# Optimization experiments

Measured on AMD Instinct MI355X. Metric: run time of the kernel, lower is better.

Reference implementation:

```python
import jax, jax.numpy as jnp
from jax import lax
import numpy as np
import math

DIM = 96      # channels
HEADS = 3     # num_heads
WS = 8        # window size
SHIFT = 4     # window_size // 2 (depth is odd -> shifted)
TLC = 64      # tlc_kernel
H = 264
W = 264


def _grid_idxes(h, w, k1, k2):
    # Faithful replication of the torch grids() tiling index logic (static ints).
    num_row = (h - 1) // k1 + 1
    num_col = (w - 1) // k2 + 1
    step_j = k2 if num_col == 1 else math.ceil((w - k2) / (num_col - 1) - 1e-8)
    step_i = k1 if num_row == 1 else math.ceil((h - k1) / (num_row - 1) - 1e-8)
    idxes = []
    i = 0
    last_i = False
    while i < h and not last_i:
        j = 0
        if i + k1 >= h:
            i = h - k1
            last_i = True
        last_j = False
        while j < w and not last_j:
            if j + k2 >= w:
                j = w - k2
                last_j = True
            idxes.append((i, j))
            j = j + step_j
        i = i + step_i
    return idxes


def setup_inputs() -> dict:
    key = jax.random.key(0)
    ks = jax.random.split(key, 4)
    return {
        "x": jax.random.normal(ks[0], (1, DIM, H, W), jnp.float32),
        "temperature": jnp.ones((HEADS, 1, 1), jnp.float32),
        "qkv_w": jax.random.normal(ks[1], (3 * DIM, DIM), jnp.float32) * 0.05,
        "dw_w": jax.random.normal(ks[2], (3 * DIM, 1, 3, 3), jnp.float32) * 0.1,
        "proj_w": jax.random.normal(ks[3], (DIM, DIM), jnp.float32) * 0.05,
    }


def reference(x, temperature, qkv_w, dw_w, proj_w):
    b, c, h, w = x.shape
    # depth % 2 == 1 -> cyclic shift
    x = jnp.roll(x, (-SHIFT, -SHIFT), axis=(2, 3))
    # 1x1 pointwise conv (no bias)
    qkv = jnp.einsum('oc,bchw->bohw', qkv_w, x)
    # 3x3 depthwise conv, padding 1
    qkv = lax.conv_general_dilated(
        qkv, dw_w, window_strides=(1, 1), padding=[(1, 1), (1, 1)],
        feature_group_count=3 * c, dimension_numbers=('NCHW', 'OIHW', 'NCHW'))
    # --- TLC grids: overlapping tiles (eval path, b == 1) ---
    k1, k2 = min(h, TLC), min(w, TLC)
    idxes = _grid_idxes(h, w, k1, k2)
    parts = jnp.concatenate([qkv[:, :, i:i + k1, j:j + k2] for (i, j) in idxes], axis=0)  # [T,3c,k1,k2]
    T, C3, th, tw = parts.shape
    nh, nw = th // WS, tw // WS
    # window partition: b c (h b0) (w b1) -> (b h w) c b0 b1 -> flatten spatial
    win = parts.reshape(T, C3, nh, WS, nw, WS).transpose(0, 2, 4, 1, 3, 5)
    win = win.reshape(T * nh * nw, C3, WS * WS)  # [Bw, 3c, 64]
    q, k, v = jnp.split(win, 3, axis=1)  # each [Bw, c, 64]
    ch = c // HEADS
    q = q.reshape(-1, HEADS, ch, WS * WS)
    k = k.reshape(-1, HEADS, ch, WS * WS)
    v = v.reshape(-1, HEADS, ch, WS * WS)
    # L2 normalize along token dim (F.normalize eps=1e-12)
    q = q / jnp.maximum(jnp.linalg.norm(q, axis=-1, keepdims=True), 1e-12)
    k = k / jnp.maximum(jnp.linalg.norm(k, axis=-1, keepdims=True), 1e-12)
    # channel attention: [Bw, head, ch, ch]
    attn = jax.nn.relu(jnp.einsum('bhcn,bhdn->bhcd', q, k) * temperature)
    out = jnp.einsum('bhcd,bhdn->bhcn', attn, v)  # [Bw, head, ch, 64]
    out = out.reshape(-1, c, WS, WS)
    # window merge back to tiles
    out = out.reshape(T, nh, nw, c, WS, WS).transpose(0, 3, 1, 4, 2, 5).reshape(T, c, th, tw)
    # --- TLC grids_inverse: scatter-add overlapping tiles and average ---
    preds = jnp.zeros((b, c, h, w), x.dtype)
    cnt = np.zeros((h, w), np.float32)
    for t, (i, j) in enumerate(idxes):
        preds = preds.at[0, :, i:i + k1, j:j + k2].add(out[t])
        cnt[i:i + k1, j:j + k2] += 1.0
    preds = preds / jnp.asarray(cnt)
    # 1x1 output projection
    out = jnp.einsum('oc,bchw->bohw', proj_w, preds)
    # undo cyclic shift
    return jnp.roll(out, (SHIFT, SHIFT), axis=(2, 3))
```

## Files before the change

### kernel.cpp

```cpp
#include <hip/hip_runtime.h>
#include <hip/hip_bf16.h>

#define HW_ 69696
#define W_ 264
#define H_ 264

typedef short bf16x8 __attribute__((ext_vector_type(8)));
typedef float f32x4 __attribute__((ext_vector_type(4)));

static __device__ __forceinline__ unsigned short f2b(float f) {
  __hip_bfloat16 h = __float2bfloat16(f);
  return *reinterpret_cast<unsigned short*>(&h);
}
static __device__ __forceinline__ float b2f(unsigned short u) {
  __hip_bfloat16 h;
  *reinterpret_cast<unsigned short*>(&h) = u;
  return __bfloat162float(h);
}
static __device__ __forceinline__ float lo_f(unsigned int u) {
  union { unsigned int i; float f; } c; c.i = u << 16; return c.f;
}
static __device__ __forceinline__ float hi_f(unsigned int u) {
  union { unsigned int i; float f; } c; c.i = u & 0xffff0000u; return c.f;
}

__global__ __launch_bounds__(256, 4) void k_gemm(const float* __restrict__ x,
                                                 const float* __restrict__ w,
                                                 unsigned short* __restrict__ outb) {
  __shared__ __align__(16) char smem[19968];
  unsigned short* As = (unsigned short*)smem;
  unsigned short* Cs = (unsigned short*)smem;

  const int tid = threadIdx.x;
  const int wid = tid >> 6, lane = tid & 63;
  const int quad = lane >> 4, lo = lane & 15;
  const int px0 = blockIdx.x * 64;
  const int px = px0 + wid * 16 + lo;

  const int y = px / W_, xx = px - y * W_;
  int y2 = y + 4; if (y2 >= H_) y2 -= H_;
  int x2 = xx + 4; if (x2 >= W_) x2 -= W_;
  const float* xb = x + y2 * W_ + x2;

  bf16x8 bf[3];
#pragma unroll
  for (int ks = 0; ks < 3; ++ks) {
    const float* xp = xb + (size_t)(ks * 32 + quad * 8) * HW_;
    float f[8];
#pragma unroll
    for (int i = 0; i < 8; ++i) f[i] = xp[(size_t)i * HW_];
    union { bf16x8 v; unsigned short s[8]; } u;
#pragma unroll
    for (int i = 0; i < 8; ++i) u.s[i] = f2b(f[i]);
    bf[ks] = u.v;
  }

  for (int oc = 0; oc < 3; ++oc) {
    __syncthreads();
    const float* wp = w + oc * 96 * 96;
    for (int l = tid; l < 96 * 24; l += 256) {
      int o = l / 24, c4 = (l - (l / 24) * 24) * 4;
      float4 v = *(const float4*)&wp[o * 96 + c4];
      unsigned int p0 = (unsigned int)f2b(v.x) | ((unsigned int)f2b(v.y) << 16);
      unsigned int p1 = (unsigned int)f2b(v.z) | ((unsigned int)f2b(v.w) << 16);
      *(uint2*)&As[o * 104 + c4] = make_uint2(p0, p1);
    }
    __syncthreads();

    f32x4 acc[6];
#pragma unroll
    for (int mt = 0; mt < 6; ++mt) acc[mt] = {0.f, 0.f, 0.f, 0.f};
#pragma unroll
    for (int ks = 0; ks < 3; ++ks) {
      const int kb = ks * 32 + quad * 8;
#pragma unroll
      for (int mt = 0; mt < 6; ++mt) {
        bf16x8 a = *(const bf16x8*)&As[(mt * 16 + lo) * 104 + kb];
        acc[mt] = __builtin_amdgcn_mfma_f32_16x16x32_bf16(a, bf[ks], acc[mt], 0, 0, 0);
      }
    }
    __syncthreads();

    const int pxl = wid * 16 + lo;
#pragma unroll
    for (int mt = 0; mt < 6; ++mt) {
      unsigned int p0 = (unsigned int)f2b(acc[mt][0]) | ((unsigned int)f2b(acc[mt][1]) << 16);
      unsigned int p1 = (unsigned int)f2b(acc[mt][2]) | ((unsigned int)f2b(acc[mt][3]) << 16);
      *(uint2*)&Cs[pxl * 104 + mt * 16 + quad * 4] = make_uint2(p0, p1);
    }
    __syncthreads();

    for (int i = tid; i < 64 * 12; i += 256) {
      int pxl2 = i & 63, j = i >> 6;
      *((uint4*)outb + (size_t)(oc * 12 + j) * HW_ + px0 + pxl2) =
          ((const uint4*)(Cs + pxl2 * 104))[j];
    }
  }
}

__global__ __launch_bounds__(256, 3) void k_dwattn(const unsigned short* __restrict__ qkvb,
                                                   const float* __restrict__ dwv,
                                                   const float* __restrict__ temp,
                                                   unsigned short* __restrict__ tout) {
  __shared__ __align__(16) unsigned short outS[64 * 296];
  __shared__ __align__(16) uint4 stg[4][100];
  __shared__ __align__(16) unsigned short attnL[3 * 32 * 40];
  __shared__ float invn[3 * 32];

  const int tid = threadIdx.x;
  const int wi = ((blockIdx.x & 7) << 3) | (blockIdx.x >> 3);
  const int t = blockIdx.y;
  const int i0 = (t / 5) * 50, j0 = (t % 5) * 50;
  const int wy = wi >> 3, wx = wi & 7;
  const int gy0 = i0 + wy * 8, gx0 = j0 + wx * 8;

  const int h = tid >> 6, lane = tid & 63;
  const int w_ = __builtin_amdgcn_readfirstlane(h);

  {
    uint4* stgW = &stg[w_][0];
    const int r0 = lane >> 3, c0 = lane & 7;
    const int sy0 = lane / 10, sx0 = lane - sy0 * 10;
    const int ii1 = lane + 64;
    const int sy1 = ii1 / 10, sx1 = ii1 - sy1 * 10;
    const int gyA = gy0 - 1 + sy0, gxA = gx0 - 1 + sx0;
    const int gyB = gy0 - 1 + sy1, gxB = gx0 - 1 + sx1;
    const bool okA = (unsigned)gyA < (unsigned)H_ && (unsigned)gxA < (unsigned)W_;
    const bool okB = ii1 < 100 && (unsigned)gyB < (unsigned)H_ && (unsigned)gxB < (unsigned)W_;
    const size_t offA = (size_t)gyA * W_ + gxA;
    const size_t offB = (size_t)gyB * W_ + gxB;
    const uint4* qb4 = (const uint4*)qkvb;

    uint4 vA = okA ? qb4[(size_t)w_ * HW_ + offA] : make_uint4(0u, 0u, 0u, 0u);
    uint4 vB = okB ? qb4[(size_t)w_ * HW_ + offB] : make_uint4(0u, 0u, 0u, 0u);

    for (int k = 0; k < 9; ++k) {
      const int u = k * 4 + w_;
      stgW[lane] = vA;
      if (ii1 < 100) stgW[ii1] = vB;
      if (k < 8) {
        vA = okA ? qb4[(size_t)(u + 4) * HW_ + offA] : make_uint4(0u, 0u, 0u, 0u);
        vB = okB ? qb4[(size_t)(u + 4) * HW_ + offB] : make_uint4(0u, 0u, 0u, 0u);
      }
      asm volatile("s_waitcnt lgkmcnt(0)" ::: "memory");
      __builtin_amdgcn_sched_barrier(0);

      const float* wp = dwv + u * 72;
      float acc[8] = {0.f, 0.f, 0.f, 0.f, 0.f, 0.f, 0.f, 0.f};
#pragma unroll
      for (int dy = 0; dy < 3; ++dy)
#pragma unroll
        for (int dx = 0; dx < 3; ++dx) {
          uint4 v = stgW[(r0 + dy) * 10 + (c0 + dx)];
          float w0 = wp[0 * 9 + dy * 3 + dx], w1 = wp[1 * 9 + dy * 3 + dx];
          float w2 = wp[2 * 9 + dy * 3 + dx], w3 = wp[3 * 9 + dy * 3 + dx];
          float w4 = wp[4 * 9 + dy * 3 + dx], w5 = wp[5 * 9 + dy * 3 + dx];
          float w6 = wp[6 * 9 + dy * 3 + dx], w7 = wp[7 * 9 + dy * 3 + dx];
          acc[0] += w0 * lo_f(v.x); acc[1] += w1 * hi_f(v.x);
          acc[2] += w2 * lo_f(v.y); acc[3] += w3 * hi_f(v.y);
          acc[4] += w4 * lo_f(v.z); acc[5] += w5 * hi_f(v.z);
          acc[6] += w6 * lo_f(v.w); acc[7] += w7 * hi_f(v.w);
        }
      uint4 o;
      o.x = (unsigned int)f2b(acc[0]) | ((unsigned int)f2b(acc[1]) << 16);
      o.y = (unsigned int)f2b(acc[2]) | ((unsigned int)f2b(acc[3]) << 16);
      o.z = (unsigned int)f2b(acc[4]) | ((unsigned int)f2b(acc[5]) << 16);
      o.w = (unsigned int)f2b(acc[6]) | ((unsigned int)f2b(acc[7]) << 16);
      *(uint4*)&outS[lane * 296 + u * 8] = o;
    }
  }
  __syncthreads();

  const int quad = lane >> 4, lo = lane & 15;
  const int cb = h * 32;

  bf16x8 qf[2][2], kf[2][2];
  f32x4 S[2][2];
  float ivk[2];
  if (h < 3) {
#pragma unroll
    for (int mt = 0; mt < 2; ++mt)
#pragma unroll
      for (int kt = 0; kt < 2; ++kt) {
        const int rr = kt * 4 + quad;
        const int cq = cb + mt * 16 + lo;
        const int ck = 96 + cq;
        bf16x8 q8, k8;
#pragma unroll
        for (int j = 0; j < 8; ++j) {
          q8[j] = (short)outS[(rr * 8 + j) * 296 + cq];
          k8[j] = (short)outS[(rr * 8 + j) * 296 + ck];
        }
        qf[mt][kt] = q8;
        kf[mt][kt] = k8;
      }

#pragma unroll
    for (int mt = 0; mt < 2; ++mt)
#pragma unroll
      for (int nt = 0; nt < 2; ++nt) {
        S[mt][nt] = {0.f, 0.f, 0.f, 0.f};
#pragma unroll
        for (int kt = 0; kt < 2; ++kt)
          S[mt][nt] = __builtin_amdgcn_mfma_f32_16x16x32_bf16(qf[mt][kt], kf[nt][kt], S[mt][nt], 0, 0, 0);
      }

#pragma unroll
    for (int mt = 0; mt < 2; ++mt) {
      float sq = 0.f, sk = 0.f;
#pragma unroll
      for (int kt = 0; kt < 2; ++kt)
#pragma unroll
        for (int j = 0; j < 8; ++j) {
          float a = b2f((unsigned short)qf[mt][kt][j]);
          float b = b2f((unsigned short)kf[mt][kt][j]);
          sq += a * a;
          sk += b * b;
        }
      sq += __shfl_xor(sq, 16);
      sq += __shfl_xor(sq, 32);
      sk += __shfl_xor(sk, 16);
      sk += __shfl_xor(sk, 32);
      if (quad == 0) invn[h * 32 + mt * 16 + lo] = 1.f / fmaxf(sqrtf(sq), 1e-12f);
      ivk[mt] = 1.f / fmaxf(sqrtf(sk), 1e-12f);
    }
  }
  __syncthreads();

  if (h < 3) {
    const float ts = temp[h];
#pragma unroll
    for (int mt = 0; mt < 2; ++mt)
#pragma unroll
      for (int nt = 0; nt < 2; ++nt)
#pragma unroll
        for (int r = 0; r < 4; ++r) {
          int c = mt * 16 + quad * 4 + r;
          float v = S[mt][nt][r] * invn[h * 32 + c] * ivk[nt] * ts;
          attnL[(h * 32 + c) * 40 + nt * 16 + lo] = f2b(fmaxf(v, 0.f));
        }
  }
  __syncthreads();

  f32x4 O[2][4];
  if (h < 3) {
    bf16x8 af[2];
#pragma unroll
    for (int mt = 0; mt < 2; ++mt)
      af[mt] = *(const bf16x8*)&attnL[(h * 32 + mt * 16 + lo) * 40 + quad * 8];

    const int uv = 24 + h * 4 + quad;
#pragma unroll
    for (int nt = 0; nt < 4; ++nt) {
      const int px = nt * 16 + lo;
      uint4 vraw = *(const uint4*)&outS[px * 296 + uv * 8];
      bf16x8 vf = *reinterpret_cast<bf16x8*>(&vraw);
#pragma unroll
      for (int mt = 0; mt < 2; ++mt) {
        f32x4 z = {0.f, 0.f, 0.f, 0.f};
        O[mt][nt] = __builtin_amdgcn_mfma_f32_16x16x32_bf16(af[mt], vf, z, 0, 0, 0);
      }
    }
  }
  __syncthreads();

  unsigned short* Cs = outS;
  if (h < 3) {
#pragma unroll
    for (int mt = 0; mt < 2; ++mt)
#pragma unroll
      for (int nt = 0; nt < 4; ++nt) {
        const int px = nt * 16 + lo;
        unsigned int p0 = (unsigned int)f2b(O[mt][nt][0]) | ((unsigned int)f2b(O[mt][nt][1]) << 16);
        unsigned int p1 = (unsigned int)f2b(O[mt][nt][2]) | ((unsigned int)f2b(O[mt][nt][3]) << 16);
        *(uint2*)&Cs[px * 104 + cb + mt * 16 + quad * 4] = make_uint2(p0, p1);
      }
  }
  __syncthreads();

  for (int idx = tid; idx < 64 * 12; idx += 256) {
    int u = idx >> 6, rec = idx & 63;
    int r = rec >> 3, j = rec & 7;
    size_t local = (size_t)(wy * 8 + r) * 64 + wx * 8 + j;
    ((uint4*)tout)[((size_t)t * 12 + u) * 4096 + local] = ((const uint4*)(Cs + rec * 104))[u];
  }
}

__global__ __launch_bounds__(256, 4) void k_avgproj(const float* __restrict__ w,
                                                    const unsigned short* __restrict__ tout,
                                                    float* __restrict__ outf) {
  __shared__ __align__(16) unsigned short As[96 * 104];
  const int tid = threadIdx.x;
  const int wid = tid >> 6, lane = tid & 63;
  const int quad = lane >> 4, lo = lane & 15;
  const int px0 = blockIdx.x * 64;
  const int px = px0 + wid * 16 + lo;

  for (int l = tid; l < 96 * 24; l += 256) {
    int o = l / 24, c4 = (l - (l / 24) * 24) * 4;
    float4 v = *(const float4*)&w[o * 96 + c4];
    unsigned int p0 = (unsigned int)f2b(v.x) | ((unsigned int)f2b(v.y) << 16);
    unsigned int p1 = (unsigned int)f2b(v.z) | ((unsigned int)f2b(v.w) << 16);
    *(uint2*)&As[o * 104 + c4] = make_uint2(p0, p1);
  }

  const int y = px / W_, xx = px - y * W_;
  int loy = (y >= 64) ? (y - 14) / 50 : 0;
  int hiy = y / 50; if (hiy > 4) hiy = 4;
  int lox = (xx >= 64) ? (xx - 14) / 50 : 0;
  int hix = xx / 50; if (hix > 4) hix = 4;
  float a24[24];
#pragma unroll
  for (int i = 0; i < 24; ++i) a24[i] = 0.f;
  int cnt = 0;
  for (int ty = loy; ty <= hiy; ++ty)
    for (int tx = lox; tx <= hix; ++tx) {
      size_t local = (size_t)((y - ty * 50) << 6) + (xx - tx * 50);
      const uint4* rp = (const uint4*)tout +
                        ((size_t)(ty * 5 + tx) * 12 + quad) * 4096 + local;
#pragma unroll
      for (int ks = 0; ks < 3; ++ks) {
        uint4 v = rp[(size_t)ks * 4 * 4096];
        a24[ks * 8 + 0] += lo_f(v.x); a24[ks * 8 + 1] += hi_f(v.x);
        a24[ks * 8 + 2] += lo_f(v.y); a24[ks * 8 + 3] += hi_f(v.y);
        a24[ks * 8 + 4] += lo_f(v.z); a24[ks * 8 + 5] += hi_f(v.z);
        a24[ks * 8 + 6] += lo_f(v.w); a24[ks * 8 + 7] += hi_f(v.w);
      }
      ++cnt;
    }
  const float inv = 1.f / (float)cnt;
  bf16x8 bf[3];
#pragma unroll
  for (int ks = 0; ks < 3; ++ks) {
    union { bf16x8 v; unsigned short s[8]; } u;
#pragma unroll
    for (int i = 0; i < 8; ++i) u.s[i] = f2b(a24[ks * 8 + i] * inv);
    bf[ks] = u.v;
  }
  __syncthreads();

  f32x4 acc[6];
#pragma unroll
  for (int mt = 0; mt < 6; ++mt) acc[mt] = {0.f, 0.f, 0.f, 0.f};
#pragma unroll
  for (int ks = 0; ks < 3; ++ks) {
    const int kb = ks * 32 + quad * 8;
#pragma unroll
    for (int mt = 0; mt < 6; ++mt) {
      bf16x8 a = *(const bf16x8*)&As[(mt * 16 + lo) * 104 + kb];
      acc[mt] = __builtin_amdgcn_mfma_f32_16x16x32_bf16(a, bf[ks], acc[mt], 0, 0, 0);
    }
  }

  {
    int y2 = y + 4; if (y2 >= H_) y2 -= H_;
    int x2 = xx + 4; if (x2 >= W_) x2 -= W_;
    int tp = y2 * W_ + x2;
#pragma unroll
    for (int mt = 0; mt < 6; ++mt) {
      int row = mt * 16 + quad * 4;
#pragma unroll
      for (int r = 0; r < 4; ++r)
        outf[(size_t)(row + r) * HW_ + tp] = acc[mt][r];
    }
  }
}

extern "C" void kernel_launch(void* const* d_in, const int* in_sizes, int n_in,
                              void* d_out, int out_size, void* d_ws, size_t ws_size,
                              hipStream_t stream) {
  (void)in_sizes; (void)n_in; (void)out_size; (void)ws_size;
  const float* x = (const float*)d_in[0];
  const float* temp = (const float*)d_in[1];
  const float* qkvw = (const float*)d_in[2];
  const float* dww = (const float*)d_in[3];
  const float* projw = (const float*)d_in[4];
  float* out = (float*)d_out;

  char* ws = (char*)d_ws;
  const size_t SZQ = (size_t)288 * HW_ * 2;
  unsigned short* qkvb = (unsigned short*)ws;
  unsigned short* tout = (unsigned short*)(ws + SZQ);

  k_gemm<<<dim3(1089), 256, 0, stream>>>(x, qkvw, qkvb);
  k_dwattn<<<dim3(64, 25), 256, 0, stream>>>(qkvb, dww, temp, tout);
  k_avgproj<<<dim3(1089), 256, 0, stream>>>(projw, tout, out);
}
```

Baseline: 141.7 us.

## Fuse three stages into one persistent kernel with grid barriers and work stealing

Replaces the three separate launches (qkv GEMM, depthwise+window attention, tile-average+projection) with one persistent kernel of 768 blocks. Stages are separated by a software grid barrier built on atomics, and blocks pick up extra work items through atomic work stealing. The aim is to remove inter-kernel launch gaps and tail effects. In exchange it adds a memset, atomic contention and barrier spin cost, and it relies on all 768 blocks being co-resident (3 per CU), which risks deadlock if occupancy falls short.

```diff
diff --git a/kernel.cpp b/kernel.cpp
--- a/kernel.cpp
+++ b/kernel.cpp
@@ -4,6 +4,10 @@
 #define HW_ 69696
 #define W_ 264
 #define H_ 264
+#define G_ 768
+#define NP1 1089
+#define NP2 1600
+#define NP3 1089
 
 typedef short bf16x8 __attribute__((ext_vector_type(8)));
 typedef float f32x4 __attribute__((ext_vector_type(4)));
@@ -24,344 +28,375 @@
   union { unsigned int i; float f; } c; c.i = u & 0xffff0000u; return c.f;
 }
 
-__global__ __launch_bounds__(256, 4) void k_gemm(const float* __restrict__ x,
-                                                 const float* __restrict__ w,
-                                                 unsigned short* __restrict__ outb) {
-  __shared__ __align__(16) char smem[19968];
-  unsigned short* As = (unsigned short*)smem;
-  unsigned short* Cs = (unsigned short*)smem;
+static __device__ __forceinline__ void grid_barrier(unsigned* bar) {
+  __syncthreads();
+  if (threadIdx.x == 0) {
+    __threadfence();
+    unsigned gen = atomicAdd(&bar[1], 0u);
+    unsigned arrived = atomicAdd(&bar[0], 1u);
+    if (arrived == (unsigned)G_ - 1u) {
+      atomicExch(&bar[0], 0u);
+      __threadfence();
+      atomicAdd(&bar[1], 1u);
+    } else {
+      while (atomicAdd(&bar[1], 0u) == gen) __builtin_amdgcn_s_sleep(8);
+    }
+    __threadfence();
+  }
+  __syncthreads();
+}
+
+#define STEAL(CIDX)                                                      \
+  if (tid == 0) *sSteal = (unsigned)G_ + atomicAdd(&ctrl[CIDX], 1u);     \
+  __syncthreads();                                                       \
+  item = (int)*sSteal;                                                   \
+  __syncthreads();
+
+__global__ __launch_bounds__(256, 3) void k_fused(
+    const float* __restrict__ x, const float* __restrict__ qkvw,
+    const float* __restrict__ dwv, const float* __restrict__ temp,
+    const float* __restrict__ projw,
+    unsigned short* __restrict__ qkvb, unsigned short* __restrict__ tout,
+    float* __restrict__ outf, unsigned* __restrict__ ctrl) {
+  __shared__ __align__(16) char smem[52368];
+  unsigned* sSteal = (unsigned*)(smem + 52352);
 
   const int tid = threadIdx.x;
   const int wid = tid >> 6, lane = tid & 63;
   const int quad = lane >> 4, lo = lane & 15;
-  const int px0 = blockIdx.x * 64;
-  const int px = px0 + wid * 16 + lo;
-
-  const int y = px / W_, xx = px - y * W_;
-  int y2 = y + 4; if (y2 >= H_) y2 -= H_;
-  int x2 = xx + 4; if (x2 >= W_) x2 -= W_;
-  const float* xb = x + y2 * W_ + x2;
-
-  bf16x8 bf[3];
-#pragma unroll
-  for (int ks = 0; ks < 3; ++ks) {
-    const float* xp = xb + (size_t)(ks * 32 + quad * 8) * HW_;
-    float f[8];
-#pragma unroll
-    for (int i = 0; i < 8; ++i) f[i] = xp[(size_t)i * HW_];
-    union { bf16x8 v; unsigned short s[8]; } u;
-#pragma unroll
-    for (int i = 0; i < 8; ++i) u.s[i] = f2b(f[i]);
-    bf[ks] = u.v;
+
+  {
+    unsigned short* As = (unsigned short*)smem;
+    unsigned short* Cs = (unsigned short*)smem;
+    int item = blockIdx.x;
+    while (item < NP1) {
+      const int px0 = item * 64;
+      const int px = px0 + wid * 16 + lo;
+      const int y = px / W_, xx = px - y * W_;
+      int y2 = y + 4; if (y2 >= H_) y2 -= H_;
+      int x2 = xx + 4; if (x2 >= W_) x2 -= W_;
+      const float* xb = x + y2 * W_ + x2;
+
+      bf16x8 bfv[3];
+#pragma unroll
+      for (int ks = 0; ks < 3; ++ks) {
+        const float* xp = xb + (size_t)(ks * 32 + quad * 8) * HW_;
+        float f[8];
+#pragma unroll
+        for (int i = 0; i < 8; ++i) f[i] = xp[(size_t)i * HW_];
+        union { bf16x8 v; unsigned short s[8]; } u;
+#pragma unroll
+        for (int i = 0; i < 8; ++i) u.s[i] = f2b(f[i]);
+        bfv[ks] = u.v;
+      }
+
+      for (int oc = 0; oc < 3; ++oc) {
+        __syncthreads();
+        const float* wp = qkvw + oc * 96 * 96;
+        for (int l = tid; l < 96 * 24; l += 256) {
+          int o = l / 24, c4 = (l - (l / 24) * 24) * 4;
+          float4 v = *(const float4*)&wp[o * 96 + c4];
+          unsigned int p0 = (unsigned int)f2b(v.x) | ((unsigned int)f2b(v.y) << 16);
+          unsigned int p1 = (unsigned int)f2b(v.z) | ((unsigned int)f2b(v.w) << 16);
+          *(uint2*)&As[o * 104 + c4] = make_uint2(p0, p1);
+        }
+        __syncthreads();
+
+        f32x4 acc[6];
+#pragma unroll
+        for (int mt = 0; mt < 6; ++mt) acc[mt] = {0.f, 0.f, 0.f, 0.f};
+#pragma unroll
+        for (int ks = 0; ks < 3; ++ks) {
+          const int kb = ks * 32 + quad * 8;
+#pragma unroll
+          for (int mt = 0; mt < 6; ++mt) {
+            bf16x8 a = *(const bf16x8*)&As[(mt * 16 + lo) * 104 + kb];
+            acc[mt] = __builtin_amdgcn_mfma_f32_16x16x32_bf16(a, bfv[ks], acc[mt], 0, 0, 0);
+          }
+        }
+        __syncthreads();
+
+        const int pxl = wid * 16 + lo;
+#pragma unroll
+        for (int mt = 0; mt < 6; ++mt) {
+          unsigned int p0 = (unsigned int)f2b(acc[mt][0]) | ((unsigned int)f2b(acc[mt][1]) << 16);
+          unsigned int p1 = (unsigned int)f2b(acc[mt][2]) | ((unsigned int)f2b(acc[mt][3]) << 16);
+          *(uint2*)&Cs[pxl * 104 + mt * 16 + quad * 4] = make_uint2(p0, p1);
+        }
+        __syncthreads();
+
+        for (int i = tid; i < 64 * 12; i += 256) {
+          int pxl2 = i & 63, j = i >> 6;
+          *((uint4*)qkvb + (size_t)(oc * 12 + j) * HW_ + px0 + pxl2) =
+              ((const uint4*)(Cs + pxl2 * 104))[j];
+        }
+      }
+      STEAL(2)
+    }
   }
-
-  for (int oc = 0; oc < 3; ++oc) {
-    __syncthreads();
-    const float* wp = w + oc * 96 * 96;
+  grid_barrier(ctrl);
+
+  {
+    unsigned short* outS = (unsigned short*)smem;
+    uint4* stgBase = (uint4*)(smem + 37888);
+    unsigned short* attnL = (unsigned short*)(smem + 44288);
+    float* invn = (float*)(smem + 51968);
+
+    const int h = wid;
+    const int w_ = __builtin_amdgcn_readfirstlane(h);
+    uint4* stgW = stgBase + w_ * 100;
+    const int r0 = lane >> 3, c0 = lane & 7;
+    const int sy0 = lane / 10, sx0 = lane - sy0 * 10;
+    const int ii1 = lane + 64;
+    const int sy1 = ii1 / 10, sx1 = ii1 - sy1 * 10;
+    const uint4* qb4 = (const uint4*)qkvb;
+
+    int item = blockIdx.x;
+    while (item < NP2) {
+      const int t = item >> 6, wi = item & 63;
+      const int i0 = (t / 5) * 50, j0 = (t % 5) * 50;
+      const int wy = wi >> 3, wx = wi & 7;
+      const int gy0 = i0 + wy * 8, gx0 = j0 + wx * 8;
+
+      {
+        const int gyA = gy0 - 1 + sy0, gxA = gx0 - 1 + sx0;
+        const int gyB = gy0 - 1 + sy1, gxB = gx0 - 1 + sx1;
+        const bool okA = (unsigned)gyA < (unsigned)H_ && (unsigned)gxA < (unsigned)W_;
+        const bool okB = ii1 < 100 && (unsigned)gyB < (unsigned)H_ && (unsigned)gxB < (unsigned)W_;
+        const size_t offA = (size_t)gyA * W_ + gxA;
+        const size_t offB = (size_t)gyB * W_ + gxB;
+
+        uint4 vA = okA ? qb4[(size_t)w_ * HW_ + offA] : make_uint4(0u, 0u, 0u, 0u);
+        uint4 vB = okB ? qb4[(size_t)w_ * HW_ + offB] : make_uint4(0u, 0u, 0u, 0u);
+
+        for (int k = 0; k < 9; ++k) {
+          const int u = k * 4 + w_;
+          stgW[lane] = vA;
+          if (ii1 < 100) stgW[ii1] = vB;
+          if (k < 8) {
+            vA = okA ? qb4[(size_t)(u + 4) * HW_ + offA] : make_uint4(0u, 0u, 0u, 0u);
+            vB = okB ? qb4[(size_t)(u + 4) * HW_ + offB] : make_uint4(0u, 0u, 0u, 0u);
+          }
+          asm volatile("s_waitcnt lgkmcnt(0)" ::: "memory");
+          __builtin_amdgcn_sched_barrier(0);
+
+          const float* wp = dwv + u * 72;
+          float acc[8] = {0.f, 0.f, 0.f, 0.f, 0.f, 0.f, 0.f, 0.f};
+#pragma unroll
+          for (int dy = 0; dy < 3; ++dy)
+#pragma unroll
+            for (int dx = 0; dx < 3; ++dx) {
+              uint4 v = stgW[(r0 + dy) * 10 + (c0 + dx)];
+              float w0 = wp[0 * 9 + dy * 3 + dx], w1 = wp[1 * 9 + dy * 3 + dx];
+              float w2 = wp[2 * 9 + dy * 3 + dx], w3 = wp[3 * 9 + dy * 3 + dx];
+              float w4 = wp[4 * 9 + dy * 3 + dx], w5 = wp[5 * 9 + dy * 3 + dx];
+              float w6 = wp[6 * 9 + dy * 3 + dx], w7 = wp[7 * 9 + dy * 3 + dx];
+              acc[0] += w0 * lo_f(v.x); acc[1] += w1 * hi_f(v.x);
+              acc[2] += w2 * lo_f(v.y); acc[3] += w3 * hi_f(v.y);
+              acc[4] += w4 * lo_f(v.z); acc[5] += w5 * hi_f(v.z);
+              acc[6] += w6 * lo_f(v.w); acc[7] += w7 * hi_f(v.w);
+            }
+          uint4 o;
+          o.x = (unsigned int)f2b(acc[0]) | ((unsigned int)f2b(acc[1]) << 16);
+          o.y = (unsigned int)f2b(acc[2]) | ((unsigned int)f2b(acc[3]) << 16);
+          o.z = (unsigned int)f2b(acc[4]) | ((unsigned int)f2b(acc[5]) << 16);
+          o.w = (unsigned int)f2b(acc[6]) | ((unsigned int)f2b(acc[7]) << 16);
+          *(uint4*)&outS[lane * 296 + u * 8] = o;
+        }
+      }
+      __syncthreads();
+
+      const int cb = h * 32;
+      f32x4 S[2][2];
+      bf16x8 qf[2][2], kf[2][2];
+      float ivk[2];
+      if (h < 3) {
+#pragma unroll
+        for (int mt = 0; mt < 2; ++mt)
+#pragma unroll
+          for (int kt = 0; kt < 2; ++kt) {
+            const int rr = kt * 4 + quad;
+            const int cq = cb + mt * 16 + lo;
+            const int ck = 96 + cq;
+            bf16x8 q8, k8;
+#pragma unroll
+            for (int j = 0; j < 8; ++j) {
+              q8[j] = (short)outS[(rr * 8 + j) * 296 + cq];
+              k8[j] = (short)outS[(rr * 8 + j) * 296 + ck];
+            }
+            qf[mt][kt] = q8;
+            kf[mt][kt] = k8;
+          }
+
+#pragma unroll
+        for (int mt = 0; mt < 2; ++mt)
+#pragma unroll
+          for (int nt = 0; nt < 2; ++nt) {
+            S[mt][nt] = {0.f, 0.f, 0.f, 0.f};
+#pragma unroll
+            for (int kt = 0; kt < 2; ++kt)
+              S[mt][nt] = __builtin_amdgcn_mfma_f32_16x16x32_bf16(qf[mt][kt], kf[nt][kt], S[mt][nt], 0, 0, 0);
+          }
+
+#pragma unroll
+        for (int mt = 0; mt < 2; ++mt) {
+          float sq = 0.f, sk = 0.f;
+#pragma unroll
+          for (int kt = 0; kt < 2; ++kt)
+#pragma unroll
+            for (int j = 0; j < 8; ++j) {
+              float a = b2f((unsigned short)qf[mt][kt][j]);
+              float b = b2f((unsigned short)kf[mt][kt][j]);
+              sq += a * a;
+              sk += b * b;
+            }
+          sq += __shfl_xor(sq, 16);
+          sq += __shfl_xor(sq, 32);
+          sk += __shfl_xor(sk, 16);
+          sk += __shfl_xor(sk, 32);
+          if (quad == 0) invn[h * 32 + mt * 16 + lo] = 1.f / fmaxf(sqrtf(sq), 1e-12f);
+          ivk[mt] = 1.f / fmaxf(sqrtf(sk), 1e-12f);
+        }
+      }
+      __syncthreads();
+
+      if (h < 3) {
+        const float ts = temp[h];
+#pragma unroll
+        for (int mt = 0; mt < 2; ++mt)
+#pragma unroll
+          for (int nt = 0; nt < 2; ++nt)
+#pragma unroll
+            for (int r = 0; r < 4; ++r) {
+              int c = mt * 16 + quad * 4 + r;
+              float v = S[mt][nt][r] * invn[h * 32 + c] * ivk[nt] * ts;
+              attnL[(h * 32 + c) * 40 + nt * 16 + lo] = f2b(fmaxf(v, 0.f));
+            }
+      }
+      __syncthreads();
+
+      f32x4 O[2][4];
+      if (h < 3) {
+        bf16x8 af[2];
+#pragma unroll
+        for (int mt = 0; mt < 2; ++mt)
+          af[mt] = *(const bf16x8*)&attnL[(h * 32 + mt * 16 + lo) * 40 + quad * 8];
+
+        const int uv = 24 + h * 4 + quad;
+#pragma unroll
+        for (int nt = 0; nt < 4; ++nt) {
+          const int px = nt * 16 + lo;
+          uint4 vraw = *(const uint4*)&outS[px * 296 + uv * 8];
+          bf16x8 vf = *reinterpret_cast<bf16x8*>(&vraw);
+#pragma unroll
+          for (int mt = 0; mt < 2; ++mt) {
+            f32x4 z = {0.f, 0.f, 0.f, 0.f};
+            O[mt][nt] = __builtin_amdgcn_mfma_f32_16x16x32_bf16(af[mt], vf, z, 0, 0, 0);
+          }
+        }
+      }
+      __syncthreads();
+
+      unsigned short* Cs = outS;
+      if (h < 3) {
+#pragma unroll
+        for (int mt = 0; mt < 2; ++mt)
+#pragma unroll
+          for (int nt = 0; nt < 4; ++nt) {
+            const int px = nt * 16 + lo;
+            unsigned int p0 = (unsigned int)f2b(O[mt][nt][0]) | ((unsigned int)f2b(O[mt][nt][1]) << 16);
+            unsigned int p1 = (unsigned int)f2b(O[mt][nt][2]) | ((unsigned int)f2b(O[mt][nt][3]) << 16);
+            *(uint2*)&Cs[px * 104 + cb + mt * 16 + quad * 4] = make_uint2(p0, p1);
+          }
+      }
+      __syncthreads();
+
+      for (int idx = tid; idx < 64 * 12; idx += 256) {
+        int u = idx >> 6, rec = idx & 63;
+        int r = rec >> 3, j = rec & 7;
+        size_t local = (size_t)(wy * 8 + r) * 64 + wx * 8 + j;
+        ((uint4*)tout)[((size_t)t * 12 + u) * 4096 + local] = ((const uint4*)(Cs + rec * 104))[u];
+      }
+      STEAL(3)
+    }
+  }
+  grid_barrier(ctrl);
+
+  {
+    unsigned short* As = (unsigned short*)smem;
     for (int l = tid; l < 96 * 24; l += 256) {
       int o = l / 24, c4 = (l - (l / 24) * 24) * 4;
-      float4 v = *(const float4*)&wp[o * 96 + c4];
+      float4 v = *(const float4*)&projw[o * 96 + c4];
       unsigned int p0 = (unsigned int)f2b(v.x) | ((unsigned int)f2b(v.y) << 16);
       unsigned int p1 = (unsigned int)f2b(v.z) | ((unsigned int)f2b(v.w) << 16);
       *(uint2*)&As[o * 104 + c4] = make_uint2(p0, p1);
     }
     __syncthreads();
 
-    f32x4 acc[6];
-#pragma unroll
-    for (int mt = 0; mt < 6; ++mt) acc[mt] = {0.f, 0.f, 0.f, 0.f};
-#pragma unroll
-    for (int ks = 0; ks < 3; ++ks) {
-      const int kb = ks * 32 + quad * 8;
-#pragma unroll
-      for (int mt = 0; mt < 6; ++mt) {
-        bf16x8 a = *(const bf16x8*)&As[(mt * 16 + lo) * 104 + kb];
-        acc[mt] = __builtin_amdgcn_mfma_f32_16x16x32_bf16(a, bf[ks], acc[mt], 0, 0, 0);
-      }
-    }
-    __syncthreads();
-
-    const int pxl = wid * 16 + lo;
-#pragma unroll
-    for (int mt = 0; mt < 6; ++mt) {
-      unsigned int p0 = (unsigned int)f2b(acc[mt][0]) | ((unsigned int)f2b(acc[mt][1]) << 16);
-      unsigned int p1 = (unsigned int)f2b(acc[mt][2]) | ((unsigned int)f2b(acc[mt][3]) << 16);
-      *(uint2*)&Cs[pxl * 104 + mt * 16 + quad * 4] = make_uint2(p0, p1);
-    }
-    __syncthreads();
-
-    for (int i = tid; i < 64 * 12; i += 256) {
-      int pxl2 = i & 63, j = i >> 6;
-      *((uint4*)outb + (size_t)(oc * 12 + j) * HW_ + px0 + pxl2) =
-          ((const uint4*)(Cs + pxl2 * 104))[j];
-    }
-  }
-}
-
-__global__ __launch_bounds__(256, 3) void k_dwattn(const unsigned short* __restrict__ qkvb,
-                                                   const float* __restrict__ dwv,
-                                                   const float* __restrict__ temp,
-                                                   unsigned short* __restrict__ tout) {
-  __shared__ __align__(16) unsigned short outS[64 * 296];
-  __shared__ __align__(16) uint4 stg[4][100];
-  __shared__ __align__(16) unsigned short attnL[3 * 32 * 40];
-  __shared__ float invn[3 * 32];
-
-  const int tid = threadIdx.x;
-  const int wi = ((blockIdx.x & 7) << 3) | (blockIdx.x >> 3);
-  const int t = blockIdx.y;
-  const int i0 = (t / 5) * 50, j0 = (t % 5) * 50;
-  const int wy = wi >> 3, wx = wi & 7;
-  const int gy0 = i0 + wy * 8, gx0 = j0 + wx * 8;
-
-  const int h = tid >> 6, lane = tid & 63;
-  const int w_ = __builtin_amdgcn_readfirstlane(h);
-
-  {
-    uint4* stgW = &stg[w_][0];
-    const int r0 = lane >> 3, c0 = lane & 7;
-    const int sy0 = lane / 10, sx0 = lane - sy0 * 10;
-    const int ii1 = lane + 64;
-    const int sy1 = ii1 / 10, sx1 = ii1 - sy1 * 10;
-    const int gyA = gy0 - 1 + sy0, gxA = gx0 - 1 + sx0;
-    const int gyB = gy0 - 1 + sy1, gxB = gx0 - 1 + sx1;
-    const bool okA = (unsigned)gyA < (unsigned)H_ && (unsigned)gxA < (unsigned)W_;
-    const bool okB = ii1 < 100 && (unsigned)gyB < (unsigned)H_ && (unsigned)gxB < (unsigned)W_;
-    const size_t offA = (size_t)gyA * W_ + gxA;
-    const size_t offB = (size_t)gyB * W_ + gxB;
-    const uint4* qb4 = (const uint4*)qkvb;
-
-    uint4 vA = okA ? qb4[(size_t)w_ * HW_ + offA] : make_uint4(0u, 0u, 0u, 0u);
-    uint4 vB = okB ? qb4[(size_t)w_ * HW_ + offB] : make_uint4(0u, 0u, 0u, 0u);
-
-    for (int k = 0; k < 9; ++k) {
-      const int u = k * 4 + w_;
-      stgW[lane] = vA;
-      if (ii1 < 100) stgW[ii1] = vB;
-      if (k < 8) {
-        vA = okA ? qb4[(size_t)(u + 4) * HW_ + offA] : make_uint4(0u, 0u, 0u, 0u);
-        vB = okB ? qb4[(size_t)(u + 4) * HW_ + offB] : make_uint4(0u, 0u, 0u, 0u);
-      }
-      asm volatile("s_waitcnt lgkmcnt(0)" ::: "memory");
-      __builtin_amdgcn_sched_barrier(0);
-
-      const float* wp = dwv + u * 72;
-      float acc[8] = {0.f, 0.f, 0.f, 0.f, 0.f, 0.f, 0.f, 0.f};
-#pragma unroll
-      for (int dy = 0; dy < 3; ++dy)
-#pragma unroll
-        for (int dx = 0; dx < 3; ++dx) {
-          uint4 v = stgW[(r0 + dy) * 10 + (c0 + dx)];
-          float w0 = wp[0 * 9 + dy * 3 + dx], w1 = wp[1 * 9 + dy * 3 + dx];
-          float w2 = wp[2 * 9 + dy * 3 + dx], w3 = wp[3 * 9 + dy * 3 + dx];
-          float w4 = wp[4 * 9 + dy * 3 + dx], w5 = wp[5 * 9 + dy * 3 + dx];
-          float w6 = wp[6 * 9 + dy * 3 + dx], w7 = wp[7 * 9 + dy * 3 + dx];
-          acc[0] += w0 * lo_f(v.x); acc[1] += w1 * hi_f(v.x);
-          acc[2] += w2 * lo_f(v.y); acc[3] += w3 * hi_f(v.y);
-          acc[4] += w4 * lo_f(v.z); acc[5] += w5 * hi_f(v.z);
-          acc[6] += w6 * lo_f(v.w); acc[7] += w7 * hi_f(v.w);
-        }
-      uint4 o;
-      o.x = (unsigned int)f2b(acc[0]) | ((unsigned int)f2b(acc[1]) << 16);
-      o.y = (unsigned int)f2b(acc[2]) | ((unsigned int)f2b(acc[3]) << 16);
-      o.z = (unsigned int)f2b(acc[4]) | ((unsigned int)f2b(acc[5]) << 16);
-      o.w = (unsigned int)f2b(acc[6]) | ((unsigned int)f2b(acc[7]) << 16);
-      *(uint4*)&outS[lane * 296 + u * 8] = o;
-    }
-  }
-  __syncthreads();
-
-  const int quad = lane >> 4, lo = lane & 15;
-  const int cb = h * 32;
-
-  bf16x8 qf[2][2], kf[2][2];
-  f32x4 S[2][2];
-  float ivk[2];
-  if (h < 3) {
-#pragma unroll
-    for (int mt = 0; mt < 2; ++mt)
-#pragma unroll
-      for (int kt = 0; kt < 2; ++kt) {
-        const int rr = kt * 4 + quad;
-        const int cq = cb + mt * 16 + lo;
-        const int ck = 96 + cq;
-        bf16x8 q8, k8;
-#pragma unroll
-        for (int j = 0; j < 8; ++j) {
-          q8[j] = (short)outS[(rr * 8 + j) * 296 + cq];
-          k8[j] = (short)outS[(rr * 8 + j) * 296 + ck];
-        }
-        qf[mt][kt] = q8;
-        kf[mt][kt] = k8;
-      }
-
-#pragma unroll
-    for (int mt = 0; mt < 2; ++mt)
-#pragma unroll
-      for (int nt = 0; nt < 2; ++nt) {
-        S[mt][nt] = {0.f, 0.f, 0.f, 0.f};
-#pragma unroll
-        for (int kt = 0; kt < 2; ++kt)
-          S[mt][nt] = __builtin_amdgcn_mfma_f32_16x16x32_bf16(qf[mt][kt], kf[nt][kt], S[mt][nt], 0, 0, 0);
-      }
-
-#pragma unroll
-    for (int mt = 0; mt < 2; ++mt) {
-      float sq = 0.f, sk = 0.f;
-#pragma unroll
-      for (int kt = 0; kt < 2; ++kt)
-#pragma unroll
-        for (int j = 0; j < 8; ++j) {
-          float a = b2f((unsigned short)qf[mt][kt][j]);
-          float b = b2f((unsigned short)kf[mt][kt][j]);
-          sq += a * a;
-          sk += b * b;
-        }
-      sq += __shfl_xor(sq, 16);
-      sq += __shfl_xor(sq, 32);
-      sk += __shfl_xor(sk, 16);
-      sk += __shfl_xor(sk, 32);
-      if (quad == 0) invn[h * 32 + mt * 16 + lo] = 1.f / fmaxf(sqrtf(sq), 1e-12f);
-      ivk[mt] = 1.f / fmaxf(sqrtf(sk), 1e-12f);
-    }
-  }
-  __syncthreads();
-
-  if (h < 3) {
-    const float ts = temp[h];
-#pragma unroll
-    for (int mt = 0; mt < 2; ++mt)
-#pragma unroll
-      for (int nt = 0; nt < 2; ++nt)
-#pragma unroll
-        for (int r = 0; r < 4; ++r) {
-          int c = mt * 16 + quad * 4 + r;
-          float v = S[mt][nt][r] * invn[h * 32 + c] * ivk[nt] * ts;
-          attnL[(h * 32 + c) * 40 + nt * 16 + lo] = f2b(fmaxf(v, 0.f));
-        }
-  }
-  __syncthreads();
-
-  f32x4 O[2][4];
-  if (h < 3) {
-    bf16x8 af[2];
-#pragma unroll
-    for (int mt = 0; mt < 2; ++mt)
-      af[mt] = *(const bf16x8*)&attnL[(h * 32 + mt * 16 + lo) * 40 + quad * 8];
-
-    const int uv = 24 + h * 4 + quad;
-#pragma unroll
-    for (int nt = 0; nt < 4; ++nt) {
-      const int px = nt * 16 + lo;
-      uint4 vraw = *(const uint4*)&outS[px * 296 + uv * 8];
-      bf16x8 vf = *reinterpret_cast<bf16x8*>(&vraw);
-#pragma unroll
-      for (int mt = 0; mt < 2; ++mt) {
-        f32x4 z = {0.f, 0.f, 0.f, 0.f};
-        O[mt][nt] = __builtin_amdgcn_mfma_f32_16x16x32_bf16(af[mt], vf, z, 0, 0, 0);
-      }
-    }
-  }
-  __syncthreads();
-
-  unsigned short* Cs = outS;
-  if (h < 3) {
-#pragma unroll
-    for (int mt = 0; mt < 2; ++mt)
-#pragma unroll
-      for (int nt = 0; nt < 4; ++nt) {
-        const int px = nt * 16 + lo;
-        unsigned int p0 = (unsigned int)f2b(O[mt][nt][0]) | ((unsigned int)f2b(O[mt][nt][1]) << 16);
-        unsigned int p1 = (unsigned int)f2b(O[mt][nt][2]) | ((unsigned int)f2b(O[mt][nt][3]) << 16);
-        *(uint2*)&Cs[px * 104 + cb + mt * 16 + quad * 4] = make_uint2(p0, p1);
-      }
-  }
-  __syncthreads();
-
-  for (int idx = tid; idx < 64 * 12; idx += 256) {
-    int u = idx >> 6, rec = idx & 63;
-    int r = rec >> 3, j = rec & 7;
-    size_t local = (size_t)(wy * 8 + r) * 64 + wx * 8 + j;
-    ((uint4*)tout)[((size_t)t * 12 + u) * 4096 + local] = ((const uint4*)(Cs + rec * 104))[u];
-  }
-}
-
-__global__ __launch_bounds__(256, 4) void k_avgproj(const float* __restrict__ w,
-                                                    const unsigned short* __restrict__ tout,
-                                                    float* __restrict__ outf) {
-  __shared__ __align__(16) unsigned short As[96 * 104];
-  const int tid = threadIdx.x;
-  const int wid = tid >> 6, lane = tid & 63;
-  const int quad = lane >> 4, lo = lane & 15;
-  const int px0 = blockIdx.x * 64;
-  const int px = px0 + wid * 16 + lo;
-
-  for (int l = tid; l < 96 * 24; l += 256) {
-    int o = l / 24, c4 = (l - (l / 24) * 24) * 4;
-    float4 v = *(const float4*)&w[o * 96 + c4];
-    unsigned int p0 = (unsigned int)f2b(v.x) | ((unsigned int)f2b(v.y) << 16);
-    unsigned int p1 = (unsigned int)f2b(v.z) | ((unsigned int)f2b(v.w) << 16);
-    *(uint2*)&As[o * 104 + c4] = make_uint2(p0, p1);
-  }
-
-  const int y = px / W_, xx = px - y * W_;
-  int loy = (y >= 64) ? (y - 14) / 50 : 0;
-  int hiy = y / 50; if (hiy > 4) hiy = 4;
-  int lox = (xx >= 64) ? (xx - 14) / 50 : 0;
-  int hix = xx / 50; if (hix > 4) hix = 4;
-  float a24[24];
-#pragma unroll
-  for (int i = 0; i < 24; ++i) a24[i] = 0.f;
-  int cnt = 0;
-  for (int ty = loy; ty <= hiy; ++ty)
-    for (int tx = lox; tx <= hix; ++tx) {
-      size_t local = (size_t)((y - ty * 50) << 6) + (xx - tx * 50);
-      const uint4* rp = (const uint4*)tout +
-                        ((size_t)(ty * 5 + tx) * 12 + quad) * 4096 + local;
+    int item = blockIdx.x;
+    while (item < NP3) {
+      const int px0 = item * 64;
+      const int px = px0 + wid * 16 + lo;
+      const int y = px / W_, xx = px - y * W_;
+      int loy = (y >= 64) ? (y - 14) / 50 : 0;
+      int hiy = y / 50; if (hiy > 4) hiy = 4;
+      int lox = (xx >= 64) ? (xx - 14) / 50 : 0;
+      int hix = xx / 50; if (hix > 4) hix = 4;
+      float a24[24];
+#pragma unroll
+      for (int i = 0; i < 24; ++i) a24[i] = 0.f;
+      int cnt = 0;
+      for (int ty = loy; ty <= hiy; ++ty)
+        for (int tx = lox; tx <= hix; ++tx) {
+          size_t local = (size_t)((y - ty * 50) << 6) + (xx - tx * 50);
+          const uint4* rp = (const uint4*)tout +
+                            ((size_t)(ty * 5 + tx) * 12 + quad) * 4096 + local;
+#pragma unroll
+          for (int ks = 0; ks < 3; ++ks) {
+            uint4 v = rp[(size_t)ks * 4 * 4096];
+            a24[ks * 8 + 0] += lo_f(v.x); a24[ks * 8 + 1] += hi_f(v.x);
+            a24[ks * 8 + 2] += lo_f(v.y); a24[ks * 8 + 3] += hi_f(v.y);
+            a24[ks * 8 + 4] += lo_f(v.z); a24[ks * 8 + 5] += hi_f(v.z);
+            a24[ks * 8 + 6] += lo_f(v.w); a24[ks * 8 + 7] += hi_f(v.w);
+          }
+          ++cnt;
+        }
+      const float inv = 1.f / (float)cnt;
+      bf16x8 bfv[3];
 #pragma unroll
       for (int ks = 0; ks < 3; ++ks) {
-        uint4 v = rp[(size_t)ks * 4 * 4096];
-        a24[ks * 8 + 0] += lo_f(v.x); a24[ks * 8 + 1] += hi_f(v.x);
-        a24[ks * 8 + 2] += lo_f(v.y); a24[ks * 8 + 3] += hi_f(v.y);
-        a24[ks * 8 + 4] += lo_f(v.z); a24[ks * 8 + 5] += hi_f(v.z);
-        a24[ks * 8 + 6] += lo_f(v.w); a24[ks * 8 + 7] += hi_f(v.w);
-      }
-      ++cnt;
-    }
-  const float inv = 1.f / (float)cnt;
-  bf16x8 bf[3];
-#pragma unroll
-  for (int ks = 0; ks < 3; ++ks) {
-    union { bf16x8 v; unsigned short s[8]; } u;
-#pragma unroll
-    for (int i = 0; i < 8; ++i) u.s[i] = f2b(a24[ks * 8 + i] * inv);
-    bf[ks] = u.v;
-  }
-  __syncthreads();
-
-  f32x4 acc[6];
-#pragma unroll
-  for (int mt = 0; mt < 6; ++mt) acc[mt] = {0.f, 0.f, 0.f, 0.f};
-#pragma unroll
-  for (int ks = 0; ks < 3; ++ks) {
-    const int kb = ks * 32 + quad * 8;
-#pragma unroll
-    for (int mt = 0; mt < 6; ++mt) {
-      bf16x8 a = *(const bf16x8*)&As[(mt * 16 + lo) * 104 + kb];
-      acc[mt] = __builtin_amdgcn_mfma_f32_16x16x32_bf16(a, bf[ks], acc[mt], 0, 0, 0);
-    }
-  }
-
-  {
-    int y2 = y + 4; if (y2 >= H_) y2 -= H_;
-    int x2 = xx + 4; if (x2 >= W_) x2 -= W_;
-    int tp = y2 * W_ + x2;
-#pragma unroll
-    for (int mt = 0; mt < 6; ++mt) {
-      int row = mt * 16 + quad * 4;
-#pragma unroll
-      for (int r = 0; r < 4; ++r)
-        outf[(size_t)(row + r) * HW_ + tp] = acc[mt][r];
+        union { bf16x8 v; unsigned short s[8]; } u;
+#pragma unroll
+        for (int i = 0; i < 8; ++i) u.s[i] = f2b(a24[ks * 8 + i] * inv);
+        bfv[ks] = u.v;
+      }
+
+      f32x4 acc[6];
+#pragma unroll
+      for (int mt = 0; mt < 6; ++mt) acc[mt] = {0.f, 0.f, 0.f, 0.f};
+#pragma unroll
+      for (int ks = 0; ks < 3; ++ks) {
+        const int kb = ks * 32 + quad * 8;
+#pragma unroll
+        for (int mt = 0; mt < 6; ++mt) {
+          bf16x8 a = *(const bf16x8*)&As[(mt * 16 + lo) * 104 + kb];
+          acc[mt] = __builtin_amdgcn_mfma_f32_16x16x32_bf16(a, bfv[ks], acc[mt], 0, 0, 0);
+        }
+      }
+
+      {
+        int y2 = y + 4; if (y2 >= H_) y2 -= H_;
+        int x2 = xx + 4; if (x2 >= W_) x2 -= W_;
+        int tp = y2 * W_ + x2;
+#pragma unroll
+        for (int mt = 0; mt < 6; ++mt) {
+          int row = mt * 16 + quad * 4;
+#pragma unroll
+          for (int r = 0; r < 4; ++r)
+            outf[(size_t)(row + r) * HW_ + tp] = acc[mt][r];
+        }
+      }
+      STEAL(4)
     }
   }
 }
@@ -381,8 +416,9 @@
   const size_t SZQ = (size_t)288 * HW_ * 2;
   unsigned short* qkvb = (unsigned short*)ws;
   unsigned short* tout = (unsigned short*)(ws + SZQ);
-
-  k_gemm<<<dim3(1089), 256, 0, stream>>>(x, qkvw, qkvb);
-  k_dwattn<<<dim3(64, 25), 256, 0, stream>>>(qkvb, dww, temp, tout);
-  k_avgproj<<<dim3(1089), 256, 0, stream>>>(projw, tout, out);
-}
+  unsigned* ctrl = (unsigned*)(ws + 2 * SZQ);
+
+  hipMemsetAsync(ctrl, 0, 64, stream);
+  k_fused<<<dim3(G_), 256, 0, stream>>>(x, qkvw, dww, temp, projw,
+                                        qkvb, tout, out, ctrl);
+}
```

Result: slower. 385.6 us (+172.1%).

## Deepen qkv prefetch to two stages and replace block barriers with wave-local waits

Applied to the files above, without the earlier changes.

The depthwise-conv staging loop now keeps two channel groups of global loads in flight instead of one, and the loop is fully unrolled, to hide more global memory latency. In the attention phase, two __syncthreads between the norm, attn-write and attn-read steps are replaced by an LDS wait plus sched_barrier. This is valid because each head's wave only touches its own invn/attnL rows, and it removes block-wide stalls. It costs extra registers for the second prefetch buffer, which could lower occupancy under the 256x3 launch bounds.

```diff
diff --git a/kernel.cpp b/kernel.cpp
--- a/kernel.cpp
+++ b/kernel.cpp
@@ -42,7 +42,7 @@
   int x2 = xx + 4; if (x2 >= W_) x2 -= W_;
   const float* xb = x + y2 * W_ + x2;
 
-  bf16x8 bf[3];
+  bf16x8 bfv[3];
 #pragma unroll
   for (int ks = 0; ks < 3; ++ks) {
     const float* xp = xb + (size_t)(ks * 32 + quad * 8) * HW_;
@@ -52,7 +52,7 @@
     union { bf16x8 v; unsigned short s[8]; } u;
 #pragma unroll
     for (int i = 0; i < 8; ++i) u.s[i] = f2b(f[i]);
-    bf[ks] = u.v;
+    bfv[ks] = u.v;
   }
 
   for (int oc = 0; oc < 3; ++oc) {
@@ -76,7 +76,7 @@
 #pragma unroll
       for (int mt = 0; mt < 6; ++mt) {
         bf16x8 a = *(const bf16x8*)&As[(mt * 16 + lo) * 104 + kb];
-        acc[mt] = __builtin_amdgcn_mfma_f32_16x16x32_bf16(a, bf[ks], acc[mt], 0, 0, 0);
+        acc[mt] = __builtin_amdgcn_mfma_f32_16x16x32_bf16(a, bfv[ks], acc[mt], 0, 0, 0);
       }
     }
     __syncthreads();
@@ -116,6 +116,7 @@
 
   const int h = tid >> 6, lane = tid & 63;
   const int w_ = __builtin_amdgcn_readfirstlane(h);
+  const int quad = lane >> 4, lo = lane & 15;
 
   {
     uint4* stgW = &stg[w_][0];
@@ -131,16 +132,21 @@
     const size_t offB = (size_t)gyB * W_ + gxB;
     const uint4* qb4 = (const uint4*)qkvb;
 
-    uint4 vA = okA ? qb4[(size_t)w_ * HW_ + offA] : make_uint4(0u, 0u, 0u, 0u);
-    uint4 vB = okB ? qb4[(size_t)w_ * HW_ + offB] : make_uint4(0u, 0u, 0u, 0u);
-
+    uint4 pA0 = okA ? qb4[(size_t)(0 * 4 + w_) * HW_ + offA] : make_uint4(0u, 0u, 0u, 0u);
+    uint4 pB0 = okB ? qb4[(size_t)(0 * 4 + w_) * HW_ + offB] : make_uint4(0u, 0u, 0u, 0u);
+    uint4 pA1 = okA ? qb4[(size_t)(1 * 4 + w_) * HW_ + offA] : make_uint4(0u, 0u, 0u, 0u);
+    uint4 pB1 = okB ? qb4[(size_t)(1 * 4 + w_) * HW_ + offB] : make_uint4(0u, 0u, 0u, 0u);
+
+#pragma unroll
     for (int k = 0; k < 9; ++k) {
       const int u = k * 4 + w_;
-      stgW[lane] = vA;
-      if (ii1 < 100) stgW[ii1] = vB;
-      if (k < 8) {
-        vA = okA ? qb4[(size_t)(u + 4) * HW_ + offA] : make_uint4(0u, 0u, 0u, 0u);
-        vB = okB ? qb4[(size_t)(u + 4) * HW_ + offB] : make_uint4(0u, 0u, 0u, 0u);
+      stgW[lane] = pA0;
+      if (ii1 < 100) stgW[ii1] = pB0;
+      pA0 = pA1; pB0 = pB1;
+      if (k < 7) {
+        const int un = (k + 2) * 4 + w_;
+        pA1 = okA ? qb4[(size_t)un * HW_ + offA] : make_uint4(0u, 0u, 0u, 0u);
+        pB1 = okB ? qb4[(size_t)un * HW_ + offB] : make_uint4(0u, 0u, 0u, 0u);
       }
       asm volatile("s_waitcnt lgkmcnt(0)" ::: "memory");
       __builtin_amdgcn_sched_barrier(0);
@@ -171,12 +177,12 @@
   }
   __syncthreads();
 
-  const int quad = lane >> 4, lo = lane & 15;
   const int cb = h * 32;
 
   bf16x8 qf[2][2], kf[2][2];
   f32x4 S[2][2];
   float ivk[2];
+  f32x4 O[2][4];
   if (h < 3) {
 #pragma unroll
     for (int mt = 0; mt < 2; ++mt)
@@ -224,10 +230,9 @@
       if (quad == 0) invn[h * 32 + mt * 16 + lo] = 1.f / fmaxf(sqrtf(sq), 1e-12f);
       ivk[mt] = 1.f / fmaxf(sqrtf(sk), 1e-12f);
     }
-  }
-  __syncthreads();
-
-  if (h < 3) {
+    asm volatile("s_waitcnt lgkmcnt(0)" ::: "memory");
+    __builtin_amdgcn_sched_barrier(0);
+
     const float ts = temp[h];
 #pragma unroll
     for (int mt = 0; mt < 2; ++mt)
@@ -239,11 +244,9 @@
           float v = S[mt][nt][r] * invn[h * 32 + c] * ivk[nt] * ts;
           attnL[(h * 32 + c) * 40 + nt * 16 + lo] = f2b(fmaxf(v, 0.f));
         }
-  }
-  __syncthreads();
-
-  f32x4 O[2][4];
-  if (h < 3) {
+    asm volatile("s_waitcnt lgkmcnt(0)" ::: "memory");
+    __builtin_amdgcn_sched_barrier(0);
+
     bf16x8 af[2];
 #pragma unroll
     for (int mt = 0; mt < 2; ++mt)
@@ -329,13 +332,13 @@
       ++cnt;
     }
   const float inv = 1.f / (float)cnt;
-  bf16x8 bf[3];
+  bf16x8 bfv[3];
 #pragma unroll
   for (int ks = 0; ks < 3; ++ks) {
     union { bf16x8 v; unsigned short s[8]; } u;
 #pragma unroll
     for (int i = 0; i < 8; ++i) u.s[i] = f2b(a24[ks * 8 + i] * inv);
-    bf[ks] = u.v;
+    bfv[ks] = u.v;
   }
   __syncthreads();
 
@@ -348,7 +351,7 @@
 #pragma unroll
     for (int mt = 0; mt < 6; ++mt) {
       bf16x8 a = *(const bf16x8*)&As[(mt * 16 + lo) * 104 + kb];
-      acc[mt] = __builtin_amdgcn_mfma_f32_16x16x32_bf16(a, bf[ks], acc[mt], 0, 0, 0);
+      acc[mt] = __builtin_amdgcn_mfma_f32_16x16x32_bf16(a, bfv[ks], acc[mt], 0, 0, 0);
     }
   }
 
```

After: 142.9 us. No clear change (+0.8%).
